# Performance work log

Measured on AMD Instinct MI355X. Metric: run time of the kernel, lower is better.

The kernel has to match this reference:

```python
import jax, jax.numpy as jnp
import numpy as np
import math

B, TQ, TK, D, I, H = 2, 2048, 2048, 2048, 2048, 16
HD = I // H  # head dim = 128
PAD = 128    # trailing keys treated as padding


def setup_inputs() -> dict:
    key = jax.random.key(0)
    ks = jax.random.split(key, 12)
    s_in = 1.0 / math.sqrt(D)
    s_i = 1.0 / math.sqrt(I)
    inp = {
        "query_states": jax.random.normal(ks[0], (B, TQ, D), jnp.float32),
        "kv_states": jax.random.normal(ks[1], (B, TK, D), jnp.float32),
        # pad the trailing PAD key positions (True = masked out)
        "kv_padding_mask": jnp.broadcast_to(jnp.arange(TK) >= (TK - PAD), (B, TK)),
        "Wq": jax.random.normal(ks[2], (I, D), jnp.float32) * s_in,
        "bq": jnp.zeros((I,), jnp.float32),
        "Wk": jax.random.normal(ks[3], (I, D), jnp.float32) * s_in,
        "bk": jnp.zeros((I,), jnp.float32),
        "Wv": jax.random.normal(ks[4], (I, D), jnp.float32) * s_in,
        "bv": jnp.zeros((I,), jnp.float32),
        "Wo": jax.random.normal(ks[5], (D, I), jnp.float32) * s_i,
        "bo": jnp.zeros((D,), jnp.float32),
        "gate": jnp.zeros((D,), jnp.float32),
    }
    return inp


def _split_heads(x):
    b, t, _ = x.shape
    return x.reshape(b, t, H, HD).transpose(0, 2, 1, 3)  # (B,H,T,HD)


def reference(query_states, kv_states, kv_padding_mask, Wq, bq, Wk, bk, Wv, bv, Wo, bo, gate):
    q = _split_heads(query_states @ Wq.T + bq)  # (B,H,Tq,HD)
    k = _split_heads(kv_states @ Wk.T + bk)     # (B,H,Tk,HD)
    v = _split_heads(kv_states @ Wv.T + bv)     # (B,H,Tk,HD)

    scores = jnp.einsum("bhqd,bhkd->bhqk", q, k) / jnp.sqrt(jnp.float32(HD))
    causal = jnp.triu(jnp.ones((TQ, TK), bool), k=1)  # True above diagonal
    neg_inf = jnp.float32(-jnp.inf)
    scores = jnp.where(causal[None, None, :, :], neg_inf, scores)
    scores = jnp.where(kv_padding_mask[:, None, None, :], neg_inf, scores)

    probs = jax.nn.softmax(scores, axis=-1)  # dropout p=0 -> identity
    ctx = jnp.einsum("bhqk,bhkd->bhqd", probs, v)
    ctx = ctx.transpose(0, 2, 1, 3).reshape(B, TQ, I)  # merge heads
    ctx = ctx @ Wo.T + bo
    ctx = ctx * jax.nn.sigmoid(gate)  # gated residual, gate init 0 -> 0.5
    return query_states + ctx
```

## Files before the change

kernel.cpp:

```cpp
#include <hip/hip_runtime.h>
#include <hip/hip_bf16.h>
#include <stdint.h>

#define B_N   2
#define T_Q   2048
#define T_K   2048
#define D_IN  2048
#define I_IN  2048
#define H_N   16
#define HD_N  128

using bf16 = __hip_bfloat16;
typedef short bf16x8 __attribute__((ext_vector_type(8)));
typedef float floatx4 __attribute__((ext_vector_type(4)));

__device__ __forceinline__ void async_copy16(const void* gsrc, void* ldst) {
    __builtin_amdgcn_global_load_lds(
        (const __attribute__((address_space(1))) void*)gsrc,
        (__attribute__((address_space(3))) void*)ldst, 16, 0, 0);
}

__device__ __forceinline__ floatx4 mfma_bf16(bf16x8 a, bf16x8 b, floatx4 c) {
    return __builtin_amdgcn_mfma_f32_16x16x32_bf16(a, b, c, 0, 0, 0);
}

#define XG 1048576
#define WG 524288
struct CastArgs {
    const float *s0, *s1, *s2, *s3, *s4, *s5;
    bf16 *d0, *d1, *d2, *d3, *d4, *d5;
};
__global__ void cast_all(CastArgs a) {
    int g = blockIdx.x * 256 + threadIdx.x;
    const float* src; bf16* dst; size_t off;
    if (g < XG)            { src = a.s0; dst = a.d0; off = (size_t)g * 8; }
    else if (g < 2 * XG)   { src = a.s1; dst = a.d1; off = (size_t)(g - XG) * 8; }
    else {
        int r = g - 2 * XG, s = r >> 19;
        off = (size_t)(r & (WG - 1)) * 8;
        src = (s == 0) ? a.s2 : (s == 1) ? a.s3 : (s == 2) ? a.s4 : a.s5;
        dst = (s == 0) ? a.d2 : (s == 1) ? a.d3 : (s == 2) ? a.d4 : a.d5;
    }
    float4 x = *((const float4*)(src + off));
    float4 y = *((const float4*)(src + off + 4));
    union { bf16x8 v; bf16 h[8]; } u;
    u.h[0] = __float2bfloat16(x.x); u.h[1] = __float2bfloat16(x.y);
    u.h[2] = __float2bfloat16(x.z); u.h[3] = __float2bfloat16(x.w);
    u.h[4] = __float2bfloat16(y.x); u.h[5] = __float2bfloat16(y.y);
    u.h[6] = __float2bfloat16(y.z); u.h[7] = __float2bfloat16(y.w);
    *((bf16x8*)(dst + off)) = u.v;
}


#define GEMM_SETUP(APTR, WPTR, KDIM)                                            \
    __shared__ bf16 sAls[3][256 * 64];                                          \
    __shared__ bf16 sBls[3][128 * 64];                                          \
    bf16 *aC = &sAls[0][0], *aN = &sAls[1][0], *aP = &sAls[2][0];               \
    bf16 *bC = &sBls[0][0], *bN = &sBls[1][0], *bP = &sBls[2][0];               \
    const int tid  = threadIdx.x;                                               \
    const int wave = tid >> 6, lane = tid & 63;                                 \
    const int quad = lane >> 4, r16 = lane & 15;                                \
    const int wm = wave >> 1, wn = wave & 1;                                    \
    const int K  = (KDIM);                                                      \
    const int NT = (KDIM) / 64;                                                 \
    floatx4 acc[4][4];                                                          \
    _Pragma("unroll") for (int i = 0; i < 4; i++)                               \
      _Pragma("unroll") for (int j = 0; j < 4; j++)                             \
        acc[i][j] = (floatx4)(0.0f);                                            \
    const int p0 = tid, p1 = tid + 512, p2 = tid + 1024, p3 = tid + 1536;       \
    const bf16* srcA0 = (APTR) + (size_t)(m0 + (p0 >> 3)) * K + (((p0 & 7) ^ ((p0 >> 3) & 7)) * 8); \
    const bf16* srcA1 = (APTR) + (size_t)(m0 + (p1 >> 3)) * K + (((p1 & 7) ^ ((p1 >> 3) & 7)) * 8); \
    const bf16* srcA2 = (APTR) + (size_t)(m0 + (p2 >> 3)) * K + (((p2 & 7) ^ ((p2 >> 3) & 7)) * 8); \
    const bf16* srcA3 = (APTR) + (size_t)(m0 + (p3 >> 3)) * K + (((p3 & 7) ^ ((p3 >> 3) & 7)) * 8); \
    const bf16* srcB0 = (WPTR) + (size_t)(n0 + (p0 >> 3)) * K + (((p0 & 7) ^ ((p0 >> 3) & 7)) * 8); \
    const bf16* srcB1 = (WPTR) + (size_t)(n0 + (p1 >> 3)) * K + (((p1 & 7) ^ ((p1 >> 3) & 7)) * 8); \
    const int dA0 = p0 * 8, dA1 = p1 * 8, dA2 = p2 * 8, dA3 = p3 * 8;           \
    const int dB0 = p0 * 8, dB1 = p1 * 8;                                       \
    int offA[4][2], offB[4][2];                                                 \
    _Pragma("unroll") for (int mt = 0; mt < 4; mt++)                            \
      _Pragma("unroll") for (int ks = 0; ks < 2; ks++)                          \
        offA[mt][ks] = (wm*64 + mt*16 + r16) * 64 + (((ks*4 + quad) ^ (r16 & 7)) * 8); \
    _Pragma("unroll") for (int nt = 0; nt < 4; nt++)                            \
      _Pragma("unroll") for (int ks = 0; ks < 2; ks++)                          \
        offB[nt][ks] = (wn*64 + nt*16 + r16) * 64 + (((ks*4 + quad) ^ (r16 & 7)) * 8)

#define GEMM_PROLOGUE()                                                         \
    async_copy16(srcA0,      aC + dA0);                                         \
    async_copy16(srcA1,      aC + dA1);                                         \
    async_copy16(srcA2,      aC + dA2);                                         \
    async_copy16(srcA3,      aC + dA3);                                         \
    async_copy16(srcB0,      bC + dB0);                                         \
    async_copy16(srcB1,      bC + dB1);                                         \
    async_copy16(srcA0 + 64, aN + dA0);                                         \
    async_copy16(srcA1 + 64, aN + dA1);                                         \
    async_copy16(srcA2 + 64, aN + dA2);                                         \
    async_copy16(srcA3 + 64, aN + dA3);                                         \
    async_copy16(srcB0 + 64, bN + dB0);                                         \
    async_copy16(srcB1 + 64, bN + dB1);                                         \
    asm volatile("s_waitcnt vmcnt(6)" ::: "memory");                            \
    asm volatile("s_barrier" ::: "memory")

#define GEMM_TILE_BODY()                                                        \
  do {                                                                          \
    const int kp = (t + 2) * 64;                                                \
    const bool pre = (t < NT - 2);                                              \
    bf16x8 aF[2][2], bF[4][2], aG[2][2];                                        \
    _Pragma("unroll") for (int ks = 0; ks < 2; ks++) {                          \
      aF[0][ks] = *(const bf16x8*)(aC + offA[0][ks]);                           \
      aF[1][ks] = *(const bf16x8*)(aC + offA[1][ks]);                           \
      bF[0][ks] = *(const bf16x8*)(bC + offB[0][ks]);                           \
      bF[1][ks] = *(const bf16x8*)(bC + offB[1][ks]);                           \
      bF[2][ks] = *(const bf16x8*)(bC + offB[2][ks]);                           \
      bF[3][ks] = *(const bf16x8*)(bC + offB[3][ks]);                           \
    }                                                                           \
    if (pre) {                                                                  \
      async_copy16(srcA0 + kp, aP + dA0);                                       \
      async_copy16(srcA1 + kp, aP + dA1);                                       \
      async_copy16(srcA2 + kp, aP + dA2);                                       \
    }                                                                           \
    asm volatile("s_barrier" ::: "memory");                                     \
    asm volatile("s_waitcnt lgkmcnt(0)" ::: "memory");                          \
    __builtin_amdgcn_sched_barrier(0);                                          \
    __builtin_amdgcn_s_setprio(1);                                              \
    _Pragma("unroll") for (int ks = 0; ks < 2; ks++)                            \
      _Pragma("unroll") for (int mi = 0; mi < 2; mi++)                          \
        _Pragma("unroll") for (int ni = 0; ni < 4; ni++)                        \
          acc[mi][ni] = mfma_bf16(aF[mi][ks], bF[ni][ks], acc[mi][ni]);         \
    __builtin_amdgcn_s_setprio(0);                                              \
    asm volatile("s_barrier" ::: "memory");                                     \
    _Pragma("unroll") for (int ks = 0; ks < 2; ks++) {                          \
      aG[0][ks] = *(const bf16x8*)(aC + offA[2][ks]);                           \
      aG[1][ks] = *(const bf16x8*)(aC + offA[3][ks]);                           \
    }                                                                           \
    if (pre) {                                                                  \
      async_copy16(srcA3 + kp, aP + dA3);                                       \
      async_copy16(srcB0 + kp, bP + dB0);                                       \
      async_copy16(srcB1 + kp, bP + dB1);                                       \
    }                                                                           \
    if (pre)                 asm volatile("s_waitcnt vmcnt(6)" ::: "memory");   \
    else if (t == NT - 2)    asm volatile("s_waitcnt vmcnt(0)" ::: "memory");   \
    asm volatile("s_barrier" ::: "memory");                                     \
    asm volatile("s_waitcnt lgkmcnt(0)" ::: "memory");                          \
    __builtin_amdgcn_sched_barrier(0);                                          \
    __builtin_amdgcn_s_setprio(1);                                              \
    _Pragma("unroll") for (int ks = 0; ks < 2; ks++)                            \
      _Pragma("unroll") for (int mi = 0; mi < 2; mi++)                          \
        _Pragma("unroll") for (int ni = 0; ni < 4; ni++)                        \
          acc[2+mi][ni] = mfma_bf16(aG[mi][ks], bF[ni][ks], acc[2+mi][ni]);     \
    __builtin_amdgcn_s_setprio(0);                                              \
    asm volatile("s_barrier" ::: "memory");                                     \
    bf16* tmpA = aC; aC = aN; aN = aP; aP = tmpA;                               \
    bf16* tmpB = bC; bC = bN; bN = bP; bP = tmpB;                               \
  } while (0)

__global__ __launch_bounds__(512, 2) void qkv_gemm(
    const bf16* __restrict__ xq, const bf16* __restrict__ xkv,
    const bf16* __restrict__ wq, const bf16* __restrict__ wk, const bf16* __restrict__ wv,
    const float* __restrict__ bq, const float* __restrict__ bk, const float* __restrict__ bv,
    bf16* __restrict__ qo, bf16* __restrict__ ko, bf16* __restrict__ vt)
{
    const int m0  = blockIdx.x * 256;
    const int seg = blockIdx.y >> 4;
    const int n0  = (blockIdx.y & 15) * 128;
    const bf16*  Ag   = (seg == 0) ? xq : xkv;
    const bf16*  Wg   = (seg == 0) ? wq : (seg == 1) ? wk : wv;
    const float* bias = (seg == 0) ? bq : (seg == 1) ? bk : bv;

    GEMM_SETUP(Ag, Wg, D_IN);
    GEMM_PROLOGUE();
    for (int t = 0; t < NT; t++) GEMM_TILE_BODY();

    if (seg < 2) {
        bf16* Cb = (seg == 0) ? qo : ko;
        #pragma unroll
        for (int mt = 0; mt < 4; mt++)
            #pragma unroll
            for (int nt = 0; nt < 4; nt++) {
                int col = n0 + wn*64 + nt*16 + r16;
                float bs = bias[col];
                #pragma unroll
                for (int r = 0; r < 4; r++) {
                    size_t row = (size_t)(m0 + wm*64 + mt*16 + quad*4 + r);
                    Cb[row*I_IN + col] = __float2bfloat16(acc[mt][nt][r] + bs);
                }
            }
    } else {
        #pragma unroll
        for (int mt = 0; mt < 4; mt++)
            #pragma unroll
            for (int nt = 0; nt < 4; nt++) {
                int col = n0 + wn*64 + nt*16 + r16;
                float bs = bias[col];
                int hh = col >> 7, dd = col & 127;
                int m  = m0 + wm*64 + mt*16 + quad*4;
                int bb = m >> 11, tt = m & 2047;
                union { ushort4 u; bf16 h[4]; } pk;
                #pragma unroll
                for (int r = 0; r < 4; r++) pk.h[r] = __float2bfloat16(acc[mt][nt][r] + bs);
                *((ushort4*)(vt + ((size_t)((bb*16 + hh)*128 + dd))*T_K + tt)) = pk.u;
            }
    }
}

__global__ __launch_bounds__(256, 2) void flash_attn(
    const bf16* __restrict__ Q,
    const bf16* __restrict__ Km,
    const bf16* __restrict__ Vt,
    bf16* __restrict__ Ctx)
{
    __shared__ bf16 sK[2][64 * 128];
    __shared__ bf16 sV[2][128 * 64];
    __shared__ bf16 sP[64 * 80];

    const int tid  = threadIdx.x;
    const int wave = tid >> 6, lane = tid & 63;
    const int quad = lane >> 4, r16 = lane & 15;
    const int n  = blockIdx.x;
    const int bh = n & 31, qt = 31 - (n >> 5);
    const int b  = bh >> 4, h = bh & 15;

    const bf16* Qbase = Q + ((size_t)(b*T_Q) + qt*64 + wave*16) * I_IN + h*HD_N;
    bf16x8 qf[4];
    #pragma unroll
    for (int ks = 0; ks < 4; ks++)
        qf[ks] = *(const bf16x8*)(Qbase + (size_t)r16*I_IN + ks*32 + quad*8);

    floatx4 acc_o[8];
    #pragma unroll
    for (int nt = 0; nt < 8; nt++) acc_o[nt] = (floatx4)(0.0f);
    float m2[4], l[4];
    #pragma unroll
    for (int r = 0; r < 4; r++) { m2[r] = -3.0e38f; l[r] = 0.0f; }

    const int kend = (qt < 29) ? qt : 29;
    const bf16* Kb0 = Km + (size_t)(b*T_K) * I_IN + h*HD_N;
    const bf16* Vb0 = Vt + (size_t)bh * HD_N * T_K;
    const float c1 = 0.08838834764831845f * 1.4426950408889634f;

    {
        #pragma unroll
        for (int i = 0; i < 4; i++) {
            int c = wave*256 + i*64 + lane;
            int row = c >> 4, cc = (c & 15) ^ (row & 15);
            async_copy16(Kb0 + (size_t)row*I_IN + cc*8, &sK[0][c*8]);
        }
        #pragma unroll
        for (int i = 0; i < 4; i++) {
            int c = wave*256 + i*64 + lane;
            int row = c >> 3, cc = (c & 7) ^ (row & 7);
            async_copy16(Vb0 + (size_t)row*T_K + cc*8, &sV[0][c*8]);
        }
    }

    for (int kt = 0; kt <= kend; kt++) {
        const int cur = kt & 1;
        if (kt < kend) {
            const int nxt = cur ^ 1;
            #pragma unroll
            for (int i = 0; i < 4; i++) {
                int c = wave*256 + i*64 + lane;
                int row = c >> 4, cc = (c & 15) ^ (row & 15);
                async_copy16(Kb0 + (size_t)((kt+1)*64 + row)*I_IN + cc*8, &sK[nxt][c*8]);
            }
            #pragma unroll
            for (int i = 0; i < 4; i++) {
                int c = wave*256 + i*64 + lane;
                int row = c >> 3, cc = (c & 7) ^ (row & 7);
                async_copy16(Vb0 + (size_t)row*T_K + (kt+1)*64 + cc*8, &sV[nxt][c*8]);
            }
            asm volatile("s_waitcnt vmcnt(8)\n\ts_barrier" ::: "memory");
        } else {
            asm volatile("s_waitcnt vmcnt(0)\n\ts_barrier" ::: "memory");
        }

        floatx4 sacc[4];
        #pragma unroll
        for (int nt = 0; nt < 4; nt++) sacc[nt] = (floatx4)(0.0f);
        #pragma unroll
        for (int ks = 0; ks < 4; ks++) {
            bf16x8 bk[4];
            #pragma unroll
            for (int nt = 0; nt < 4; nt++) {
                int key = nt*16 + r16;
                int cc  = (ks*4 + quad) ^ r16;
                bk[nt] = *(const bf16x8*)(&sK[cur][key*128 + cc*8]);
            }
            #pragma unroll
            for (int nt = 0; nt < 4; nt++)
                sacc[nt] = mfma_bf16(qf[ks], bk[nt], sacc[nt]);
        }

        const bool diag = (kt == qt);
        float tv[4][4];
        #pragma unroll
        for (int nt = 0; nt < 4; nt++)
            #pragma unroll
            for (int r = 0; r < 4; r++) {
                float v = sacc[nt][r] * c1;
                if (diag && (nt*16 + r16 > wave*16 + quad*4 + r)) v = -1.0e30f;
                tv[nt][r] = v;
            }

        #pragma unroll
        for (int r = 0; r < 4; r++) {
            float mx = tv[0][r];
            #pragma unroll
            for (int nt = 1; nt < 4; nt++) mx = fmaxf(mx, tv[nt][r]);
            mx = fmaxf(mx, __shfl_xor(mx, 1, 64));
            mx = fmaxf(mx, __shfl_xor(mx, 2, 64));
            mx = fmaxf(mx, __shfl_xor(mx, 4, 64));
            mx = fmaxf(mx, __shfl_xor(mx, 8, 64));
            float mn = fmaxf(m2[r], mx);
            float alpha = exp2f(m2[r] - mn);
            m2[r] = mn;
            float rs = 0.0f;
            int prow = wave*16 + quad*4 + r;
            #pragma unroll
            for (int nt = 0; nt < 4; nt++) {
                float p = exp2f(tv[nt][r] - mn);
                rs += p;
                sP[prow*80 + nt*16 + r16] = __float2bfloat16(p);
            }
            rs += __shfl_xor(rs, 1, 64);
            rs += __shfl_xor(rs, 2, 64);
            rs += __shfl_xor(rs, 4, 64);
            rs += __shfl_xor(rs, 8, 64);
            l[r] = l[r]*alpha + rs;
            #pragma unroll
            for (int nt = 0; nt < 8; nt++) acc_o[nt][r] *= alpha;
        }

        #pragma unroll
        for (int ks2 = 0; ks2 < 2; ks2++) {
            bf16x8 ap = *(const bf16x8*)(&sP[(wave*16 + r16)*80 + ks2*32 + quad*8]);
            #pragma unroll
            for (int nt = 0; nt < 8; nt++) {
                int d  = nt*16 + r16;
                int cc = (ks2*4 + quad) ^ (d & 7);
                bf16x8 bv = *(const bf16x8*)(&sV[cur][d*64 + cc*8]);
                acc_o[nt] = mfma_bf16(ap, bv, acc_o[nt]);
            }
        }

        asm volatile("s_waitcnt lgkmcnt(0)\n\ts_barrier" ::: "memory");
    }

    bf16* Cb = Ctx + ((size_t)(b*T_Q) + qt*64 + wave*16) * I_IN + h*HD_N;
    #pragma unroll
    for (int r = 0; r < 4; r++) {
        float inv = 1.0f / l[r];
        #pragma unroll
        for (int nt = 0; nt < 8; nt++)
            Cb[(size_t)(quad*4 + r)*I_IN + nt*16 + r16] =
                __float2bfloat16(acc_o[nt][r] * inv);
    }
}

__global__ __launch_bounds__(512, 2) void gemm_final(
    const bf16* __restrict__ A, const bf16* __restrict__ W,
    const float* __restrict__ bias, const float* __restrict__ gate,
    const float* __restrict__ resid, float* __restrict__ Cf)
{
    const int m0 = blockIdx.x * 256;
    const int n0 = blockIdx.y * 128;

    GEMM_SETUP(A, W, I_IN);
    GEMM_PROLOGUE();
    for (int t = 0; t < NT; t++) GEMM_TILE_BODY();

    const int N = D_IN;
    #pragma unroll
    for (int mt = 0; mt < 4; mt++)
        #pragma unroll
        for (int nt = 0; nt < 4; nt++) {
            int col = n0 + wn*64 + nt*16 + r16;
            float bs = bias[col];
            float g  = gate[col];
            float sg = 1.0f / (1.0f + exp2f(-g * 1.4426950408889634f));
            #pragma unroll
            for (int r = 0; r < 4; r++) {
                size_t row = (size_t)(m0 + wm*64 + mt*16 + quad*4 + r);
                Cf[row*N + col] = resid[row*N + col] + sg * (acc[mt][nt][r] + bs);
            }
        }
}

extern "C" void kernel_launch(void* const* d_in, const int* in_sizes, int n_in,
                              void* d_out, int out_size, void* d_ws, size_t ws_size,
                              hipStream_t stream)
{
    const float* qs   = (const float*)d_in[0];
    const float* kvs  = (const float*)d_in[1];
    const float* Wq   = (const float*)d_in[3];
    const float* bq   = (const float*)d_in[4];
    const float* Wk   = (const float*)d_in[5];
    const float* bk   = (const float*)d_in[6];
    const float* Wv   = (const float*)d_in[7];
    const float* bv   = (const float*)d_in[8];
    const float* Wo   = (const float*)d_in[9];
    const float* bo   = (const float*)d_in[10];
    const float* gate = (const float*)d_in[11];
    float* out = (float*)d_out;

    bf16* ws = (bf16*)d_ws;
    const size_t WSZ = (size_t)I_IN * D_IN;
    const size_t XSZ = (size_t)B_N * T_Q * D_IN;
    bf16* wq_b  = ws;
    bf16* wk_b  = wq_b + WSZ;
    bf16* wv_b  = wk_b + WSZ;
    bf16* wo_b  = wv_b + WSZ;
    bf16* xq_b  = wo_b + WSZ;
    bf16* xkv_b = xq_b + XSZ;
    bf16* q_b   = xkv_b + XSZ;
    bf16* k_b   = q_b + XSZ;
    bf16* vt_b  = k_b + XSZ;
    bf16* ctx_b = xq_b;

    CastArgs ca;
    ca.s0 = qs;  ca.d0 = xq_b;
    ca.s1 = kvs; ca.d1 = xkv_b;
    ca.s2 = Wq;  ca.d2 = wq_b;
    ca.s3 = Wk;  ca.d3 = wk_b;
    ca.s4 = Wv;  ca.d4 = wv_b;
    ca.s5 = Wo;  ca.d5 = wo_b;
    cast_all<<<16384, 256, 0, stream>>>(ca);

    qkv_gemm<<<dim3(16, 48), 512, 0, stream>>>(xq_b, xkv_b, wq_b, wk_b, wv_b,
                                               bq, bk, bv, q_b, k_b, vt_b);

    flash_attn<<<1024, 256, 0, stream>>>(q_b, k_b, vt_b, ctx_b);

    gemm_final<<<dim3(16, 16), 512, 0, stream>>>(ctx_b, wo_b, bo, gate, qs, out);
}
```

Baseline: 419.7 us.

## Simplify GEMM tile loop to one barrier with full-fragment loads per tile

Replaces the split-phase GEMM tile body with a single-phase schedule. The old body used two half-tile MFMA groups, four barriers, sched_barrier and setprio hints. Now each tile waits on its data, issues one barrier and the next prefetch, loads all A/B fragments, then runs all 32 MFMAs. This aims to cut barrier and synchronisation overhead per K-step. In exchange it loses the interleaving of LDS reads with MFMA issue and the priority hints, and it holds twice as many A fragments live under a 512-thread, 2-block launch bound, which risks register spills.

```diff
diff --git a/kernel.cpp b/kernel.cpp
--- a/kernel.cpp
+++ b/kernel.cpp
@@ -96,59 +96,33 @@
     async_copy16(srcA2 + 64, aN + dA2);                                         \
     async_copy16(srcA3 + 64, aN + dA3);                                         \
     async_copy16(srcB0 + 64, bN + dB0);                                         \
-    async_copy16(srcB1 + 64, bN + dB1);                                         \
-    asm volatile("s_waitcnt vmcnt(6)" ::: "memory");                            \
-    asm volatile("s_barrier" ::: "memory")
+    async_copy16(srcB1 + 64, bN + dB1)
 
 #define GEMM_TILE_BODY()                                                        \
   do {                                                                          \
-    const int kp = (t + 2) * 64;                                                \
-    const bool pre = (t < NT - 2);                                              \
-    bf16x8 aF[2][2], bF[4][2], aG[2][2];                                        \
-    _Pragma("unroll") for (int ks = 0; ks < 2; ks++) {                          \
-      aF[0][ks] = *(const bf16x8*)(aC + offA[0][ks]);                           \
-      aF[1][ks] = *(const bf16x8*)(aC + offA[1][ks]);                           \
-      bF[0][ks] = *(const bf16x8*)(bC + offB[0][ks]);                           \
-      bF[1][ks] = *(const bf16x8*)(bC + offB[1][ks]);                           \
-      bF[2][ks] = *(const bf16x8*)(bC + offB[2][ks]);                           \
-      bF[3][ks] = *(const bf16x8*)(bC + offB[3][ks]);                           \
-    }                                                                           \
-    if (pre) {                                                                  \
+    if (t < NT - 1) asm volatile("s_waitcnt vmcnt(6)" ::: "memory");            \
+    else            asm volatile("s_waitcnt vmcnt(0)" ::: "memory");            \
+    asm volatile("s_barrier" ::: "memory");                                     \
+    if (t < NT - 2) {                                                           \
+      const int kp = (t + 2) * 64;                                              \
       async_copy16(srcA0 + kp, aP + dA0);                                       \
       async_copy16(srcA1 + kp, aP + dA1);                                       \
       async_copy16(srcA2 + kp, aP + dA2);                                       \
-    }                                                                           \
-    asm volatile("s_barrier" ::: "memory");                                     \
-    asm volatile("s_waitcnt lgkmcnt(0)" ::: "memory");                          \
-    __builtin_amdgcn_sched_barrier(0);                                          \
-    __builtin_amdgcn_s_setprio(1);                                              \
-    _Pragma("unroll") for (int ks = 0; ks < 2; ks++)                            \
-      _Pragma("unroll") for (int mi = 0; mi < 2; mi++)                          \
-        _Pragma("unroll") for (int ni = 0; ni < 4; ni++)                        \
-          acc[mi][ni] = mfma_bf16(aF[mi][ks], bF[ni][ks], acc[mi][ni]);         \
-    __builtin_amdgcn_s_setprio(0);                                              \
-    asm volatile("s_barrier" ::: "memory");                                     \
-    _Pragma("unroll") for (int ks = 0; ks < 2; ks++) {                          \
-      aG[0][ks] = *(const bf16x8*)(aC + offA[2][ks]);                           \
-      aG[1][ks] = *(const bf16x8*)(aC + offA[3][ks]);                           \
-    }                                                                           \
-    if (pre) {                                                                  \
       async_copy16(srcA3 + kp, aP + dA3);                                       \
       async_copy16(srcB0 + kp, bP + dB0);                                       \
       async_copy16(srcB1 + kp, bP + dB1);                                       \
     }                                                                           \
-    if (pre)                 asm volatile("s_waitcnt vmcnt(6)" ::: "memory");   \
-    else if (t == NT - 2)    asm volatile("s_waitcnt vmcnt(0)" ::: "memory");   \
-    asm volatile("s_barrier" ::: "memory");                                     \
-    asm volatile("s_waitcnt lgkmcnt(0)" ::: "memory");                          \
-    __builtin_amdgcn_sched_barrier(0);                                          \
-    __builtin_amdgcn_s_setprio(1);                                              \
+    bf16x8 aF[4][2], bF[4][2];                                                  \
+    _Pragma("unroll") for (int mt = 0; mt < 4; mt++)                            \
+      _Pragma("unroll") for (int ks = 0; ks < 2; ks++)                          \
+        aF[mt][ks] = *(const bf16x8*)(aC + offA[mt][ks]);                       \
+    _Pragma("unroll") for (int nt = 0; nt < 4; nt++)                            \
+      _Pragma("unroll") for (int ks = 0; ks < 2; ks++)                          \
+        bF[nt][ks] = *(const bf16x8*)(bC + offB[nt][ks]);                       \
     _Pragma("unroll") for (int ks = 0; ks < 2; ks++)                            \
-      _Pragma("unroll") for (int mi = 0; mi < 2; mi++)                          \
-        _Pragma("unroll") for (int ni = 0; ni < 4; ni++)                        \
-          acc[2+mi][ni] = mfma_bf16(aG[mi][ks], bF[ni][ks], acc[2+mi][ni]);     \
-    __builtin_amdgcn_s_setprio(0);                                              \
-    asm volatile("s_barrier" ::: "memory");                                     \
+      _Pragma("unroll") for (int mt = 0; mt < 4; mt++)                          \
+        _Pragma("unroll") for (int nt = 0; nt < 4; nt++)                        \
+          acc[mt][nt] = mfma_bf16(aF[mt][ks], bF[nt][ks], acc[mt][nt]);         \
     bf16* tmpA = aC; aC = aN; aN = aP; aP = tmpA;                               \
     bf16* tmpB = bC; bC = bN; bN = bP; bP = tmpB;                               \
   } while (0)
```

Result: slower. 447.1 us (+6.5%).

## Enlarge QKV GEMM tile to 256x256 and add lazy softmax rescaling

Applied to the files above, without the earlier changes.

The QKV projection GEMM is rewritten with 256x256 output tiles (8 waves in a 2x4 layout, each computing 128x64) and a double-buffered LDS pipeline that issues global-to-LDS copies between MFMA groups, halving the grid. The goal is higher arithmetic intensity and fewer redundant operand loads per output. Separately, flash attention now skips the running-max update and accumulator rescale unless some row's max grows by more than 8 (in log2 units), trading the exp and multiply work for larger intermediate exponent values. The bigger tile uses more registers and LDS (128 KB per block), which may reduce occupancy.

```diff
diff --git a/kernel.cpp b/kernel.cpp
--- a/kernel.cpp
+++ b/kernel.cpp
@@ -51,6 +51,180 @@
     *((bf16x8*)(dst + off)) = u.v;
 }
 
+
+#define QKV_READS_B(buf)                                                        \
+    _Pragma("unroll") for (int nt = 0; nt < 4; nt++) {                          \
+        bfr[nt][0] = *(const bf16x8*)(&sB[buf][offB[nt][0]]);                   \
+        bfr[nt][1] = *(const bf16x8*)(&sB[buf][offB[nt][1]]);                   \
+    }
+
+#define QKV_READS_A(buf, mtb)                                                   \
+    afr[0][0] = *(const bf16x8*)(&sA[buf][offA[(mtb)][0]]);                     \
+    afr[0][1] = *(const bf16x8*)(&sA[buf][offA[(mtb)][1]]);                     \
+    afr[1][0] = *(const bf16x8*)(&sA[buf][offA[(mtb)+1][0]]);                   \
+    afr[1][1] = *(const bf16x8*)(&sA[buf][offA[(mtb)+1][1]]);
+
+#define QKV_MFMA(mtb)                                                           \
+    asm volatile("s_waitcnt lgkmcnt(0)" ::: "memory");                          \
+    __builtin_amdgcn_sched_barrier(0);                                          \
+    __builtin_amdgcn_s_setprio(1);                                              \
+    _Pragma("unroll") for (int ks = 0; ks < 2; ks++)                            \
+      _Pragma("unroll") for (int mi = 0; mi < 2; mi++)                          \
+        _Pragma("unroll") for (int nt = 0; nt < 4; nt++)                        \
+          acc[(mtb)+mi][nt] = mfma_bf16(afr[mi][ks], bfr[nt][ks], acc[(mtb)+mi][nt]); \
+    __builtin_amdgcn_s_setprio(0);
+
+#define QKV_BAR asm volatile("s_barrier" ::: "memory")
+
+__global__ __launch_bounds__(512, 2) void qkv_gemm(
+    const bf16* __restrict__ xq, const bf16* __restrict__ xkv,
+    const bf16* __restrict__ wq, const bf16* __restrict__ wk, const bf16* __restrict__ wv,
+    const float* __restrict__ bq, const float* __restrict__ bk, const float* __restrict__ bv,
+    bf16* __restrict__ qo, bf16* __restrict__ ko, bf16* __restrict__ vt)
+{
+    __shared__ bf16 sA[2][256 * 64];
+    __shared__ bf16 sB[2][256 * 64];
+    const int tid  = threadIdx.x;
+    const int wave = tid >> 6, lane = tid & 63;
+    const int quad = lane >> 4, r16 = lane & 15;
+    const int wm = wave >> 2, wn = wave & 3;
+    const int m0  = blockIdx.x * 256;
+    const int seg = blockIdx.y >> 3;
+    const int n0  = (blockIdx.y & 7) * 256;
+    const int K   = D_IN;
+
+    const bf16*  Ag   = (seg == 0) ? xq : xkv;
+    const bf16*  Wg   = (seg == 0) ? wq : (seg == 1) ? wk : wv;
+    const float* bias = (seg == 0) ? bq : (seg == 1) ? bk : bv;
+
+    floatx4 acc[8][4];
+    #pragma unroll
+    for (int i = 0; i < 8; i++)
+        #pragma unroll
+        for (int j = 0; j < 4; j++) acc[i][j] = (floatx4)(0.0f);
+
+    const int pp0 = tid, pp1 = tid + 512, pp2 = tid + 1024, pp3 = tid + 1536;
+    const bf16* srcA0 = Ag + (size_t)(m0 + (pp0 >> 3)) * K + (((pp0 & 7) ^ ((pp0 >> 3) & 7)) * 8);
+    const bf16* srcA1 = Ag + (size_t)(m0 + (pp1 >> 3)) * K + (((pp1 & 7) ^ ((pp1 >> 3) & 7)) * 8);
+    const bf16* srcA2 = Ag + (size_t)(m0 + (pp2 >> 3)) * K + (((pp2 & 7) ^ ((pp2 >> 3) & 7)) * 8);
+    const bf16* srcA3 = Ag + (size_t)(m0 + (pp3 >> 3)) * K + (((pp3 & 7) ^ ((pp3 >> 3) & 7)) * 8);
+    const bf16* srcB0 = Wg + (size_t)(n0 + (pp0 >> 3)) * K + (((pp0 & 7) ^ ((pp0 >> 3) & 7)) * 8);
+    const bf16* srcB1 = Wg + (size_t)(n0 + (pp1 >> 3)) * K + (((pp1 & 7) ^ ((pp1 >> 3) & 7)) * 8);
+    const bf16* srcB2 = Wg + (size_t)(n0 + (pp2 >> 3)) * K + (((pp2 & 7) ^ ((pp2 >> 3) & 7)) * 8);
+    const bf16* srcB3 = Wg + (size_t)(n0 + (pp3 >> 3)) * K + (((pp3 & 7) ^ ((pp3 >> 3) & 7)) * 8);
+    const int d0 = pp0 * 8, d1 = pp1 * 8, d2 = pp2 * 8, d3 = pp3 * 8;
+
+    int offA[8][2], offB[4][2];
+    #pragma unroll
+    for (int mt = 0; mt < 8; mt++)
+        #pragma unroll
+        for (int ks = 0; ks < 2; ks++)
+            offA[mt][ks] = (wm*128 + mt*16 + r16) * 64 + (((ks*4 + quad) ^ (r16 & 7)) * 8);
+    #pragma unroll
+    for (int nt = 0; nt < 4; nt++)
+        #pragma unroll
+        for (int ks = 0; ks < 2; ks++)
+            offB[nt][ks] = (wn*64 + nt*16 + r16) * 64 + (((ks*4 + quad) ^ (r16 & 7)) * 8);
+
+    async_copy16(srcA0, &sA[0][d0]);
+    async_copy16(srcA1, &sA[0][d1]);
+    async_copy16(srcA2, &sA[0][d2]);
+    async_copy16(srcA3, &sA[0][d3]);
+    async_copy16(srcB0, &sB[0][d0]);
+    async_copy16(srcB1, &sB[0][d1]);
+    async_copy16(srcB2, &sB[0][d2]);
+    async_copy16(srcB3, &sB[0][d3]);
+    async_copy16(srcA0 + 64, &sA[1][d0]);
+    async_copy16(srcA2 + 64, &sA[1][d2]);
+    asm volatile("s_waitcnt vmcnt(2)" ::: "memory");
+    QKV_BAR;
+
+    const int NT2 = K / 128;
+    for (int i2 = 0; i2 < NT2; ++i2) {
+        const bool pre = (i2 < NT2 - 1);
+        const int kT1 = (2*i2 + 1) * 64;
+        const int kS0 = (2*i2 + 2) * 64;
+        const int kS1 = (2*i2 + 3) * 64;
+        bf16x8 bfr[4][2], afr[2][2];
+
+        QKV_READS_B(0); QKV_READS_A(0, 0);
+        async_copy16(srcA1 + kT1, &sA[1][d1]);
+        async_copy16(srcA3 + kT1, &sA[1][d3]);
+        async_copy16(srcB0 + kT1, &sB[1][d0]);
+        QKV_MFMA(0); QKV_BAR;
+        QKV_READS_A(0, 2);
+        async_copy16(srcB1 + kT1, &sB[1][d1]);
+        async_copy16(srcB2 + kT1, &sB[1][d2]);
+        async_copy16(srcB3 + kT1, &sB[1][d3]);
+        QKV_MFMA(2); QKV_BAR;
+        QKV_READS_A(0, 4);
+        if (pre) {
+            async_copy16(srcA0 + kS0, &sA[0][d0]);
+            async_copy16(srcA2 + kS0, &sA[0][d2]);
+        }
+        QKV_MFMA(4); QKV_BAR;
+        QKV_READS_A(0, 6);
+        QKV_MFMA(6);
+        if (pre) asm volatile("s_waitcnt vmcnt(2)" ::: "memory");
+        else     asm volatile("s_waitcnt vmcnt(0)" ::: "memory");
+        QKV_BAR;
+        QKV_READS_B(1); QKV_READS_A(1, 0);
+        if (pre) {
+            async_copy16(srcA1 + kS0, &sA[0][d1]);
+            async_copy16(srcA3 + kS0, &sA[0][d3]);
+            async_copy16(srcB0 + kS0, &sB[0][d0]);
+        }
+        QKV_MFMA(0); QKV_BAR;
+        QKV_READS_A(1, 2);
+        if (pre) {
+            async_copy16(srcB1 + kS0, &sB[0][d1]);
+            async_copy16(srcB2 + kS0, &sB[0][d2]);
+            async_copy16(srcB3 + kS0, &sB[0][d3]);
+        }
+        QKV_MFMA(2); QKV_BAR;
+        QKV_READS_A(1, 4);
+        if (pre) {
+            async_copy16(srcA0 + kS1, &sA[1][d0]);
+            async_copy16(srcA2 + kS1, &sA[1][d2]);
+        }
+        QKV_MFMA(4); QKV_BAR;
+        QKV_READS_A(1, 6);
+        QKV_MFMA(6);
+        asm volatile("s_waitcnt vmcnt(2)" ::: "memory");
+        QKV_BAR;
+    }
+
+    if (seg < 2) {
+        bf16* Cb = (seg == 0) ? qo : ko;
+        #pragma unroll
+        for (int mt = 0; mt < 8; mt++)
+            #pragma unroll
+            for (int nt = 0; nt < 4; nt++) {
+                int col = n0 + wn*64 + nt*16 + r16;
+                float bs = bias[col];
+                #pragma unroll
+                for (int r = 0; r < 4; r++) {
+                    size_t row = (size_t)(m0 + wm*128 + mt*16 + quad*4 + r);
+                    Cb[row*I_IN + col] = __float2bfloat16(acc[mt][nt][r] + bs);
+                }
+            }
+    } else {
+        #pragma unroll
+        for (int mt = 0; mt < 8; mt++)
+            #pragma unroll
+            for (int nt = 0; nt < 4; nt++) {
+                int col = n0 + wn*64 + nt*16 + r16;
+                float bs = bias[col];
+                int hh = col >> 7, dd = col & 127;
+                int m  = m0 + wm*128 + mt*16 + quad*4;
+                int bb = m >> 11, tt = m & 2047;
+                union { ushort4 u; bf16 h[4]; } pk;
+                #pragma unroll
+                for (int r = 0; r < 4; r++) pk.h[r] = __float2bfloat16(acc[mt][nt][r] + bs);
+                *((ushort4*)(vt + ((size_t)((bb*16 + hh)*128 + dd))*T_K + tt)) = pk.u;
+            }
+    }
+}
 
 #define GEMM_SETUP(APTR, WPTR, KDIM)                                            \
     __shared__ bf16 sAls[3][256 * 64];                                          \
@@ -153,55 +327,6 @@
     bf16* tmpB = bC; bC = bN; bN = bP; bP = tmpB;                               \
   } while (0)
 
-__global__ __launch_bounds__(512, 2) void qkv_gemm(
-    const bf16* __restrict__ xq, const bf16* __restrict__ xkv,
-    const bf16* __restrict__ wq, const bf16* __restrict__ wk, const bf16* __restrict__ wv,
-    const float* __restrict__ bq, const float* __restrict__ bk, const float* __restrict__ bv,
-    bf16* __restrict__ qo, bf16* __restrict__ ko, bf16* __restrict__ vt)
-{
-    const int m0  = blockIdx.x * 256;
-    const int seg = blockIdx.y >> 4;
-    const int n0  = (blockIdx.y & 15) * 128;
-    const bf16*  Ag   = (seg == 0) ? xq : xkv;
-    const bf16*  Wg   = (seg == 0) ? wq : (seg == 1) ? wk : wv;
-    const float* bias = (seg == 0) ? bq : (seg == 1) ? bk : bv;
-
-    GEMM_SETUP(Ag, Wg, D_IN);
-    GEMM_PROLOGUE();
-    for (int t = 0; t < NT; t++) GEMM_TILE_BODY();
-
-    if (seg < 2) {
-        bf16* Cb = (seg == 0) ? qo : ko;
-        #pragma unroll
-        for (int mt = 0; mt < 4; mt++)
-            #pragma unroll
-            for (int nt = 0; nt < 4; nt++) {
-                int col = n0 + wn*64 + nt*16 + r16;
-                float bs = bias[col];
-                #pragma unroll
-                for (int r = 0; r < 4; r++) {
-                    size_t row = (size_t)(m0 + wm*64 + mt*16 + quad*4 + r);
-                    Cb[row*I_IN + col] = __float2bfloat16(acc[mt][nt][r] + bs);
-                }
-            }
-    } else {
-        #pragma unroll
-        for (int mt = 0; mt < 4; mt++)
-            #pragma unroll
-            for (int nt = 0; nt < 4; nt++) {
-                int col = n0 + wn*64 + nt*16 + r16;
-                float bs = bias[col];
-                int hh = col >> 7, dd = col & 127;
-                int m  = m0 + wm*64 + mt*16 + quad*4;
-                int bb = m >> 11, tt = m & 2047;
-                union { ushort4 u; bf16 h[4]; } pk;
-                #pragma unroll
-                for (int r = 0; r < 4; r++) pk.h[r] = __float2bfloat16(acc[mt][nt][r] + bs);
-                *((ushort4*)(vt + ((size_t)((bb*16 + hh)*128 + dd))*T_K + tt)) = pk.u;
-            }
-    }
-}
-
 __global__ __launch_bounds__(256, 2) void flash_attn(
     const bf16* __restrict__ Q,
     const bf16* __restrict__ Km,
@@ -301,33 +426,60 @@
                 tv[nt][r] = v;
             }
 
+        float mx[4];
         #pragma unroll
         for (int r = 0; r < 4; r++) {
-            float mx = tv[0][r];
-            #pragma unroll
-            for (int nt = 1; nt < 4; nt++) mx = fmaxf(mx, tv[nt][r]);
-            mx = fmaxf(mx, __shfl_xor(mx, 1, 64));
-            mx = fmaxf(mx, __shfl_xor(mx, 2, 64));
-            mx = fmaxf(mx, __shfl_xor(mx, 4, 64));
-            mx = fmaxf(mx, __shfl_xor(mx, 8, 64));
-            float mn = fmaxf(m2[r], mx);
-            float alpha = exp2f(m2[r] - mn);
-            m2[r] = mn;
-            float rs = 0.0f;
-            int prow = wave*16 + quad*4 + r;
-            #pragma unroll
-            for (int nt = 0; nt < 4; nt++) {
-                float p = exp2f(tv[nt][r] - mn);
-                rs += p;
-                sP[prow*80 + nt*16 + r16] = __float2bfloat16(p);
-            }
-            rs += __shfl_xor(rs, 1, 64);
-            rs += __shfl_xor(rs, 2, 64);
-            rs += __shfl_xor(rs, 4, 64);
-            rs += __shfl_xor(rs, 8, 64);
-            l[r] = l[r]*alpha + rs;
-            #pragma unroll
-            for (int nt = 0; nt < 8; nt++) acc_o[nt][r] *= alpha;
+            float m_ = tv[0][r];
+            #pragma unroll
+            for (int nt = 1; nt < 4; nt++) m_ = fmaxf(m_, tv[nt][r]);
+            m_ = fmaxf(m_, __shfl_xor(m_, 1, 64));
+            m_ = fmaxf(m_, __shfl_xor(m_, 2, 64));
+            m_ = fmaxf(m_, __shfl_xor(m_, 4, 64));
+            m_ = fmaxf(m_, __shfl_xor(m_, 8, 64));
+            mx[r] = m_;
+        }
+
+        bool grow = (mx[0] > m2[0] + 8.0f) || (mx[1] > m2[1] + 8.0f) ||
+                    (mx[2] > m2[2] + 8.0f) || (mx[3] > m2[3] + 8.0f);
+        if (__any(grow)) {
+            #pragma unroll
+            for (int r = 0; r < 4; r++) {
+                float mn = fmaxf(m2[r], mx[r]);
+                float alpha = exp2f(m2[r] - mn);
+                m2[r] = mn;
+                float rs = 0.0f;
+                int prow = wave*16 + quad*4 + r;
+                #pragma unroll
+                for (int nt = 0; nt < 4; nt++) {
+                    float p = exp2f(tv[nt][r] - mn);
+                    rs += p;
+                    sP[prow*80 + nt*16 + r16] = __float2bfloat16(p);
+                }
+                rs += __shfl_xor(rs, 1, 64);
+                rs += __shfl_xor(rs, 2, 64);
+                rs += __shfl_xor(rs, 4, 64);
+                rs += __shfl_xor(rs, 8, 64);
+                l[r] = l[r]*alpha + rs;
+                #pragma unroll
+                for (int nt = 0; nt < 8; nt++) acc_o[nt][r] *= alpha;
+            }
+        } else {
+            #pragma unroll
+            for (int r = 0; r < 4; r++) {
+                float rs = 0.0f;
+                int prow = wave*16 + quad*4 + r;
+                #pragma unroll
+                for (int nt = 0; nt < 4; nt++) {
+                    float p = exp2f(tv[nt][r] - m2[r]);
+                    rs += p;
+                    sP[prow*80 + nt*16 + r16] = __float2bfloat16(p);
+                }
+                rs += __shfl_xor(rs, 1, 64);
+                rs += __shfl_xor(rs, 2, 64);
+                rs += __shfl_xor(rs, 4, 64);
+                rs += __shfl_xor(rs, 8, 64);
+                l[r] += rs;
+            }
         }
 
         #pragma unroll
@@ -425,7 +577,7 @@
     ca.s5 = Wo;  ca.d5 = wo_b;
     cast_all<<<16384, 256, 0, stream>>>(ca);
 
-    qkv_gemm<<<dim3(16, 48), 512, 0, stream>>>(xq_b, xkv_b, wq_b, wk_b, wv_b,
+    qkv_gemm<<<dim3(16, 24), 512, 0, stream>>>(xq_b, xkv_b, wq_b, wk_b, wv_b,
                                                bq, bk, bv, q_b, k_b, vt_b);
 
     flash_attn<<<1024, 256, 0, stream>>>(q_b, k_b, vt_b, ctx_b);
```

Result: slower. 428.5 us (+2.1%).
